# Performance work log

Hardware: AMD Instinct MI355X
Metric: run time of the kernel (lower is better)

## Reference

```python
import jax, jax.numpy as jnp
import numpy as np

NEG_SLOPE = 0.2
N_NODES = 50000


def _gat_layer(x, src, dst, invalid, W, al, ar, b):
    # x: [N, Fin]; src/dst: [E] (self-loops appended); invalid: [E] bool
    N = x.shape[0]
    H, F = al.shape
    z = (x @ W).reshape(N, H, F)                       # [N,H,F]
    el = jnp.sum(z * al[None], axis=-1)                # [N,H]
    er = jnp.sum(z * ar[None], axis=-1)                # [N,H]
    e = el[src] + er[dst]                              # [E,H]
    e = jnp.where(e > 0, e, NEG_SLOPE * e)             # LeakyReLU(0.2)
    e = jnp.where(invalid[:, None], -jnp.inf, e)       # removed self-loop edges
    # edge softmax per destination node (every node has a self-loop -> max finite)
    m = jax.ops.segment_max(e, dst, num_segments=N)    # [N,H]
    ex = jnp.exp(e - m[dst])
    ex = jnp.where(invalid[:, None], 0.0, ex)
    s = jax.ops.segment_sum(ex, dst, num_segments=N)   # [N,H]
    alpha = ex / s[dst]                                # [E,H]
    msg = z[src] * alpha[:, :, None]                   # [E,H,F]
    out = jax.ops.segment_sum(msg, dst, num_segments=N)  # [N,H,F]
    out = out + b.reshape(1, H, F)
    return jax.nn.elu(out)


def _with_self_loops(src, dst):
    N = N_NODES
    loop = jnp.arange(N, dtype=src.dtype)
    invalid = jnp.concatenate([src == dst, jnp.zeros(N, dtype=bool)])
    return jnp.concatenate([src, loop]), jnp.concatenate([dst, loop]), invalid


def setup_inputs() -> dict:
    key = jax.random.key(0)
    ks = jax.random.split(key, 12)
    N, Fin, H0, F0, H1, C = N_NODES, 256, 4, 32, 1, 40
    E = 800000
    sc = lambda k, shp, fan: jax.random.normal(k, shp, jnp.float32) * (1.0 / np.sqrt(fan))
    return {
        "x": jax.random.normal(ks[0], (N, Fin), jnp.float32),
        "src": jax.random.randint(ks[1], (E,), 0, N, jnp.int32),
        "dst": jax.random.randint(ks[2], (E,), 0, N, jnp.int32),
        "W0": sc(ks[3], (Fin, H0 * F0), Fin),
        "al0": sc(ks[4], (H0, F0), F0),
        "ar0": sc(ks[5], (H0, F0), F0),
        "b0": jnp.zeros((H0 * F0,), jnp.float32),
        "W1": sc(ks[6], (H0 * F0, H1 * C), H0 * F0),
        "al1": sc(ks[7], (H1, C), C),
        "ar1": sc(ks[8], (H1, C), C),
        "b1": jnp.zeros((C,), jnp.float32),
    }


def reference(x, src, dst, W0, al0, ar0, b0, W1, al1, ar1, b1):
    s, d, invalid = _with_self_loops(src, dst)
    h = _gat_layer(x, s, d, invalid, W0, al0, ar0, b0)   # [N,4,32]
    h = h.reshape(h.shape[0], -1)                        # flatten(1) -> [N,128]
    h = _gat_layer(h, s, d, invalid, W1, al1, ar1, b1)   # [N,1,40]
    return h.mean(axis=1)                                # mean over heads -> [N,40]
```

## Files before the change

kernel.cpp:

```cpp
#include <hip/hip_runtime.h>
#include <stdint.h>

#define NN 50000
#define EE 800000
#define CAP 48
#define NXCD 8
#define NPX 6250
#define EPB 2048
#define NCHUNK 391

typedef __bf16 bf16x8 __attribute__((ext_vector_type(8)));
typedef float  f32x4  __attribute__((ext_vector_type(4)));

__device__ __forceinline__ float bflo(unsigned int w){ union{unsigned int i;float f;}c; c.i=w<<16; return c.f; }
__device__ __forceinline__ float bfhi(unsigned int w){ union{unsigned int i;float f;}c; c.i=w&0xFFFF0000u; return c.f; }
__device__ __forceinline__ bf16x8 bf8_zero(){
  bf16x8 v;
  #pragma unroll
  for (int j=0;j<8;++j) v[j]=(__bf16)0.f;
  return v;
}

__global__ __launch_bounds__(256) void k_prepW0(const float* __restrict__ W0,
                                                __bf16* __restrict__ Wg){
  int tg = blockIdx.x*256 + threadIdx.x;
  if (tg >= 4096) return;
  int k8 = tg >> 7, n = tg & 127;
  bf16x8 v;
  #pragma unroll
  for (int j=0;j<8;++j) v[j] = (__bf16)W0[(k8*8+j)*128 + n];
  *(bf16x8*)(Wg + ((size_t)(k8*128 + n))*8) = v;
}

__global__ __launch_bounds__(256) void k_gemm0(const float* __restrict__ x,
    const __bf16* __restrict__ Wg, const float* __restrict__ al0, const float* __restrict__ ar0,
    __bf16* __restrict__ z0b, float* __restrict__ el0, float* __restrict__ er0,
    int* __restrict__ cursor, int* __restrict__ csrv){
  const int tid = threadIdx.x;
  const int wv = tid >> 6, ln = tid & 63, q = ln >> 4, mr = ln & 15;
  const int nhalf = wv & 1, mhalf = wv >> 1;
  const int m0w = blockIdx.x*64 + mhalf*32;
  const int n0w = nhalf*64;
  f32x4 acc[2][4];
  #pragma unroll
  for (int mt=0;mt<2;++mt)
    #pragma unroll
    for (int nt=0;nt<4;++nt) acc[mt][nt] = (f32x4){0.f,0.f,0.f,0.f};
  const bool av0 = (m0w + mr) < NN;
  const bool av1 = (m0w + 16 + mr) < NN;
  const float* xr0 = x + (size_t)(m0w + mr)*256;
  const float* xr1 = x + (size_t)(m0w + 16 + mr)*256;
  #pragma unroll
  for (int kc=0;kc<8;++kc){
    int ko = kc*32 + q*8;
    bf16x8 a0 = bf8_zero(), a1 = bf8_zero();
    if (av0){
      float4 p = *(const float4*)(xr0 + ko);
      float4 p2 = *(const float4*)(xr0 + ko + 4);
      a0[0]=(__bf16)p.x; a0[1]=(__bf16)p.y; a0[2]=(__bf16)p.z; a0[3]=(__bf16)p.w;
      a0[4]=(__bf16)p2.x; a0[5]=(__bf16)p2.y; a0[6]=(__bf16)p2.z; a0[7]=(__bf16)p2.w;
    }
    if (av1){
      float4 p = *(const float4*)(xr1 + ko);
      float4 p2 = *(const float4*)(xr1 + ko + 4);
      a1[0]=(__bf16)p.x; a1[1]=(__bf16)p.y; a1[2]=(__bf16)p.z; a1[3]=(__bf16)p.w;
      a1[4]=(__bf16)p2.x; a1[5]=(__bf16)p2.y; a1[6]=(__bf16)p2.z; a1[7]=(__bf16)p2.w;
    }
    const __bf16* wb = Wg + ((size_t)((kc*4+q)*128 + n0w + mr))*8;
    #pragma unroll
    for (int nt=0;nt<4;++nt){
      bf16x8 bf = *(const bf16x8*)(wb + (size_t)nt*16*8);
      acc[0][nt] = __builtin_amdgcn_mfma_f32_16x16x32_bf16(a0, bf, acc[0][nt], 0,0,0);
      acc[1][nt] = __builtin_amdgcn_mfma_f32_16x16x32_bf16(a1, bf, acc[1][nt], 0,0,0);
    }
  }
  float alv[4], arv[4];
  #pragma unroll
  for (int nt=0;nt<4;++nt){ int c = n0w + nt*16 + mr; alv[nt]=al0[c]; arv[nt]=ar0[c]; }
  #pragma unroll
  for (int mt=0;mt<2;++mt){
    #pragma unroll
    for (int r=0;r<4;++r){
      int grow = m0w + mt*16 + q*4 + r;
      if (grow < NN){
        #pragma unroll
        for (int nt=0;nt<4;++nt)
          z0b[(size_t)grow*128 + n0w + nt*16 + mr] = (__bf16)acc[mt][nt][r];
      }
      float pl0 = acc[mt][0][r]*alv[0] + acc[mt][1][r]*alv[1];
      float pr0 = acc[mt][0][r]*arv[0] + acc[mt][1][r]*arv[1];
      float pl1 = acc[mt][2][r]*alv[2] + acc[mt][3][r]*alv[3];
      float pr1 = acc[mt][2][r]*arv[2] + acc[mt][3][r]*arv[3];
      #pragma unroll
      for (int off=1; off<16; off<<=1){
        pl0 += __shfl_xor(pl0, off, 16); pr0 += __shfl_xor(pr0, off, 16);
        pl1 += __shfl_xor(pl1, off, 16); pr1 += __shfl_xor(pr1, off, 16);
      }
      if (mr==0 && grow<NN){
        el0[grow*4 + 2*nhalf]   = pl0; er0[grow*4 + 2*nhalf]   = pr0;
        el0[grow*4 + 2*nhalf+1] = pl1; er0[grow*4 + 2*nhalf+1] = pr1;
        if (nhalf==0){ csrv[(size_t)grow*CAP] = grow; cursor[grow] = 1; }
      }
    }
  }
}

__global__ __launch_bounds__(256) void k_scatter(const int* __restrict__ src,
    const int* __restrict__ dst, int* __restrict__ cursor, int* __restrict__ csrv){
  const int xcd = blockIdx.x & 7;
  const int chunk = blockIdx.x >> 3;
  const int lo = xcd*NPX, hi = lo + NPX;
  int e = chunk*EPB + threadIdx.x;
  #pragma unroll
  for (int it=0; it<EPB/256; ++it, e += 256){
    if (e < EE){
      int d = dst[e];
      if (d >= lo && d < hi){
        int s = src[e];
        unsigned int inv = (s==d) ? 0x80000000u : 0u;
        int pos = atomicAdd(&cursor[d], 1);
        csrv[(size_t)d*CAP + pos] = (int)((unsigned int)s | inv);
      }
    }
  }
}

__global__ __launch_bounds__(256) void k_agg0(const unsigned short* __restrict__ z0b,
    const float* __restrict__ el0, const float* __restrict__ er0,
    const int* __restrict__ cursor, const int* __restrict__ csrv,
    const float* __restrict__ b0, unsigned short* __restrict__ hb){
  int lane = threadIdx.x & 63;
  int i = __builtin_amdgcn_readfirstlane(blockIdx.x*4 + (threadIdx.x >> 6));
  int h1 = lane >> 4;
  int lane2 = lane << 1;
  const float erv = er0[(size_t)i*4 + h1];
  float ax=0.f, ay=0.f, s=0.f;
  int p = i*CAP, pe = p + cursor[i];
  for (; p+8<=pe; p+=8){
    int4 va = *(const int4*)(csrv + p);
    int4 vb = *(const int4*)(csrv + p + 4);
    int v[8] = {va.x,va.y,va.z,va.w,vb.x,vb.y,vb.z,vb.w};
    float el[8];
    #pragma unroll
    for (int j=0;j<8;++j) el[j] = el0[(size_t)(v[j]&0x7FFFFFFF)*4 + h1];
    unsigned int zw[8];
    #pragma unroll
    for (int j=0;j<8;++j)
      zw[j] = *(const unsigned int*)(z0b + (size_t)(v[j]&0x7FFFFFFF)*128 + lane2);
    #pragma unroll
    for (int j=0;j<8;++j){
      float e = el[j] + erv;
      e = fmaxf(e, 0.2f*e);
      float w = (v[j] < 0) ? 0.f : __expf(e);
      s += w; ax = fmaf(w, bflo(zw[j]), ax); ay = fmaf(w, bfhi(zw[j]), ay);
    }
  }
  for (; p+4<=pe; p+=4){
    int4 va = *(const int4*)(csrv + p);
    int v[4] = {va.x,va.y,va.z,va.w};
    float el[4];
    #pragma unroll
    for (int j=0;j<4;++j) el[j] = el0[(size_t)(v[j]&0x7FFFFFFF)*4 + h1];
    unsigned int zw[4];
    #pragma unroll
    for (int j=0;j<4;++j)
      zw[j] = *(const unsigned int*)(z0b + (size_t)(v[j]&0x7FFFFFFF)*128 + lane2);
    #pragma unroll
    for (int j=0;j<4;++j){
      float e = el[j] + erv;
      e = fmaxf(e, 0.2f*e);
      float w = (v[j] < 0) ? 0.f : __expf(e);
      s += w; ax = fmaf(w, bflo(zw[j]), ax); ay = fmaf(w, bfhi(zw[j]), ay);
    }
  }
  for (; p<pe; ++p){
    int v = csrv[p];
    int u = v & 0x7FFFFFFF;
    float e = el0[(size_t)u*4 + h1] + erv;
    e = fmaxf(e, 0.2f*e);
    float w = (v < 0) ? 0.f : __expf(e);
    unsigned int zw = *(const unsigned int*)(z0b + (size_t)u*128 + lane2);
    s += w; ax = fmaf(w, bflo(zw), ax); ay = fmaf(w, bfhi(zw), ay);
  }
  float inv = 1.f/s;
  float ox = ax*inv + b0[lane*2], oy = ay*inv + b0[lane*2+1];
  ox = ox>0.f?ox:__expf(ox)-1.f; oy = oy>0.f?oy:__expf(oy)-1.f;
  union { __bf16 b[2]; unsigned int u; } pk;
  pk.b[0]=(__bf16)ox; pk.b[1]=(__bf16)oy;
  *(unsigned int*)(hb + (size_t)i*128 + lane2) = pk.u;
}

__global__ __launch_bounds__(256) void k_gemm1(const __bf16* __restrict__ hb,
    const float* __restrict__ W1, const float* __restrict__ al1, const float* __restrict__ ar1,
    __bf16* __restrict__ z1b, float* __restrict__ el1, float* __restrict__ er1){
  __shared__ __bf16 Blds[16][48][8];
  const int tid = threadIdx.x;
  for (int t=tid; t<16*48*8; t+=256) (&Blds[0][0][0])[t] = (__bf16)0.f;
  __syncthreads();
  for (int t=tid; t<5120; t+=256){
    int k = t/40, n = t - k*40;
    Blds[k>>3][n][k&7] = (__bf16)W1[t];
  }
  __syncthreads();
  const int wm = tid >> 6, ln = tid & 63, q = ln >> 4, mr = ln & 15;
  const int m0 = blockIdx.x*64 + wm*16;
  const int arow = m0 + mr;
  const bool av = (arow < NN);
  f32x4 acc[3];
  #pragma unroll
  for (int nt=0;nt<3;++nt) acc[nt] = (f32x4){0.f,0.f,0.f,0.f};
  #pragma unroll
  for (int kc=0;kc<4;++kc){
    bf16x8 af = bf8_zero();
    if (av) af = *(const bf16x8*)(hb + (size_t)arow*128 + kc*32 + q*8);
    #pragma unroll
    for (int nt=0;nt<3;++nt){
      bf16x8 bf = *(const bf16x8*)&Blds[kc*4+q][nt*16+mr][0];
      acc[nt] = __builtin_amdgcn_mfma_f32_16x16x32_bf16(af, bf, acc[nt], 0,0,0);
    }
  }
  float alv[3], arv[3];
  #pragma unroll
  for (int nt=0;nt<3;++nt){
    int c = nt*16+mr;
    alv[nt] = (c<40) ? al1[c] : 0.f;
    arv[nt] = (c<40) ? ar1[c] : 0.f;
  }
  #pragma unroll
  for (int r=0;r<4;++r){
    int grow = m0 + q*4 + r;
    if (grow < NN){
      #pragma unroll
      for (int nt=0;nt<3;++nt){
        int c = nt*16+mr;
        if (c < 40) z1b[(size_t)grow*40 + c] = (__bf16)acc[nt][r];
      }
    }
    float pl = acc[0][r]*alv[0] + acc[1][r]*alv[1] + acc[2][r]*alv[2];
    float pr = acc[0][r]*arv[0] + acc[1][r]*arv[1] + acc[2][r]*arv[2];
    #pragma unroll
    for (int off=1; off<16; off<<=1){ pl += __shfl_xor(pl, off, 16); pr += __shfl_xor(pr, off, 16); }
    if (mr==0 && grow<NN){ el1[grow]=pl; er1[grow]=pr; }
  }
}

__global__ __launch_bounds__(256) void k_agg1(const unsigned short* __restrict__ z1b,
    const float* __restrict__ el1, const float* __restrict__ er1,
    const int* __restrict__ cursor, const int* __restrict__ csrv,
    const float* __restrict__ b1, float* __restrict__ out){
  int lane = threadIdx.x & 63;
  int i = __builtin_amdgcn_readfirstlane(blockIdx.x*4 + (threadIdx.x >> 6));
  int fl = (lane < 20) ? (lane<<1) : 0;
  const float erv = er1[i];
  float ax=0.f, ay=0.f, s=0.f;
  int p = i*CAP, pe = p + cursor[i];
  for (; p+8<=pe; p+=8){
    int4 va = *(const int4*)(csrv + p);
    int4 vb = *(const int4*)(csrv + p + 4);
    int v[8] = {va.x,va.y,va.z,va.w,vb.x,vb.y,vb.z,vb.w};
    float el[8];
    #pragma unroll
    for (int j=0;j<8;++j) el[j] = el1[v[j]&0x7FFFFFFF];
    unsigned int zw[8];
    #pragma unroll
    for (int j=0;j<8;++j)
      zw[j] = *(const unsigned int*)(z1b + (size_t)(v[j]&0x7FFFFFFF)*40 + fl);
    #pragma unroll
    for (int j=0;j<8;++j){
      float e = el[j] + erv;
      e = fmaxf(e, 0.2f*e);
      float w = (v[j] < 0) ? 0.f : __expf(e);
      s += w; ax = fmaf(w, bflo(zw[j]), ax); ay = fmaf(w, bfhi(zw[j]), ay);
    }
  }
  for (; p+4<=pe; p+=4){
    int4 va = *(const int4*)(csrv + p);
    int v[4] = {va.x,va.y,va.z,va.w};
    float el[4];
    #pragma unroll
    for (int j=0;j<4;++j) el[j] = el1[v[j]&0x7FFFFFFF];
    unsigned int zw[4];
    #pragma unroll
    for (int j=0;j<4;++j)
      zw[j] = *(const unsigned int*)(z1b + (size_t)(v[j]&0x7FFFFFFF)*40 + fl);
    #pragma unroll
    for (int j=0;j<4;++j){
      float e = el[j] + erv;
      e = fmaxf(e, 0.2f*e);
      float w = (v[j] < 0) ? 0.f : __expf(e);
      s += w; ax = fmaf(w, bflo(zw[j]), ax); ay = fmaf(w, bfhi(zw[j]), ay);
    }
  }
  for (; p<pe; ++p){
    int v = csrv[p];
    int u = v & 0x7FFFFFFF;
    float e = el1[u] + erv;
    e = fmaxf(e, 0.2f*e);
    float w = (v < 0) ? 0.f : __expf(e);
    unsigned int zw = *(const unsigned int*)(z1b + (size_t)u*40 + fl);
    s += w; ax = fmaf(w, bflo(zw), ax); ay = fmaf(w, bfhi(zw), ay);
  }
  if (lane < 20){
    float inv = 1.f/s;
    float ox = ax*inv + b1[lane*2], oy = ay*inv + b1[lane*2+1];
    ox = ox>0.f?ox:__expf(ox)-1.f; oy = oy>0.f?oy:__expf(oy)-1.f;
    *(float2*)(out + (size_t)i*40 + (lane<<1)) = make_float2(ox, oy);
  }
}

extern "C" void kernel_launch(void* const* d_in, const int* in_sizes, int n_in,
                              void* d_out, int out_size, void* d_ws, size_t ws_size,
                              hipStream_t stream){
  const float* x   = (const float*)d_in[0];
  const int*   src = (const int*)d_in[1];
  const int*   dst = (const int*)d_in[2];
  const float* W0  = (const float*)d_in[3];
  const float* al0 = (const float*)d_in[4];
  const float* ar0 = (const float*)d_in[5];
  const float* b0  = (const float*)d_in[6];
  const float* W1  = (const float*)d_in[7];
  const float* al1 = (const float*)d_in[8];
  const float* ar1 = (const float*)d_in[9];
  const float* b1  = (const float*)d_in[10];
  float* out = (float*)d_out;

  __bf16* z0b = (__bf16*)d_ws;
  __bf16* hb  = z0b + (size_t)NN*128;
  __bf16* z1b = hb  + (size_t)NN*128;
  __bf16* Wg  = z1b + (size_t)NN*40;
  float* el0 = (float*)(Wg + 32768);
  float* er0 = el0 + (size_t)NN*4;
  float* el1 = er0 + (size_t)NN*4;
  float* er1 = el1 + NN;
  int* cursor = (int*)(er1 + NN);
  int* csrv   = cursor + NN;

  k_prepW0 <<<16, 256, 0, stream>>>(W0, Wg);
  k_gemm0<<<(NN+63)/64, 256, 0, stream>>>(x, Wg, al0, ar0, z0b, el0, er0, cursor, csrv);
  k_scatter<<<NCHUNK*NXCD, 256, 0, stream>>>(src, dst, cursor, csrv);
  k_agg0 <<<NN/4, 256, 0, stream>>>((const unsigned short*)z0b, el0, er0, cursor, csrv, b0, (unsigned short*)hb);
  k_gemm1<<<(NN+63)/64, 256, 0, stream>>>(hb, W1, al1, ar1, z1b, el1, er1);
  k_agg1 <<<NN/4, 256, 0, stream>>>((const unsigned short*)z1b, el1, er1, cursor, csrv, b1, out);
}
```

Before: 239.4 us.

## Fuse edge scatter into layer-0 GEMM launch and move CSR init to prep

```diff
diff --git a/kernel.cpp b/kernel.cpp
--- a/kernel.cpp
+++ b/kernel.cpp
@@ -8,6 +8,7 @@
 #define NPX 6250
 #define EPB 2048
 #define NCHUNK 391
+#define GB0 782
 
 typedef __bf16 bf16x8 __attribute__((ext_vector_type(8)));
 typedef float  f32x4  __attribute__((ext_vector_type(4)));
@@ -21,21 +22,48 @@
   return v;
 }
 
-__global__ __launch_bounds__(256) void k_prepW0(const float* __restrict__ W0,
-                                                __bf16* __restrict__ Wg){
+__global__ __launch_bounds__(256) void k_prep(const float* __restrict__ W0,
+                                              __bf16* __restrict__ Wg,
+                                              int* __restrict__ cursor,
+                                              int* __restrict__ csrv){
   int tg = blockIdx.x*256 + threadIdx.x;
-  if (tg >= 4096) return;
-  int k8 = tg >> 7, n = tg & 127;
-  bf16x8 v;
-  #pragma unroll
-  for (int j=0;j<8;++j) v[j] = (__bf16)W0[(k8*8+j)*128 + n];
-  *(bf16x8*)(Wg + ((size_t)(k8*128 + n))*8) = v;
-}
-
-__global__ __launch_bounds__(256) void k_gemm0(const float* __restrict__ x,
+  if (tg < 4096){
+    int k8 = tg >> 7, n = tg & 127;
+    bf16x8 v;
+    #pragma unroll
+    for (int j=0;j<8;++j) v[j] = (__bf16)W0[(k8*8+j)*128 + n];
+    *(bf16x8*)(Wg + ((size_t)(k8*128 + n))*8) = v;
+  }
+  if (tg < NN){
+    cursor[tg] = 1;
+    csrv[(size_t)tg*CAP] = tg;
+  }
+}
+
+__global__ __launch_bounds__(256) void k_gemm0_scatter(const float* __restrict__ x,
     const __bf16* __restrict__ Wg, const float* __restrict__ al0, const float* __restrict__ ar0,
     __bf16* __restrict__ z0b, float* __restrict__ el0, float* __restrict__ er0,
+    const int* __restrict__ src, const int* __restrict__ dst,
     int* __restrict__ cursor, int* __restrict__ csrv){
+  if (blockIdx.x >= GB0){
+    const int xcd = blockIdx.x & 7;
+    const int chunk = (blockIdx.x - GB0) >> 3;
+    const int lo = xcd*NPX, hi = lo + NPX;
+    int e = chunk*EPB + threadIdx.x;
+    #pragma unroll
+    for (int it=0; it<EPB/256; ++it, e += 256){
+      if (e < EE){
+        int d = dst[e];
+        if (d >= lo && d < hi){
+          int s = src[e];
+          unsigned int inv = (s==d) ? 0x80000000u : 0u;
+          int pos = atomicAdd(&cursor[d], 1);
+          csrv[(size_t)d*CAP + pos] = (int)((unsigned int)s | inv);
+        }
+      }
+    }
+    return;
+  }
   const int tid = threadIdx.x;
   const int wv = tid >> 6, ln = tid & 63, q = ln >> 4, mr = ln & 15;
   const int nhalf = wv & 1, mhalf = wv >> 1;
@@ -99,27 +127,6 @@
       if (mr==0 && grow<NN){
         el0[grow*4 + 2*nhalf]   = pl0; er0[grow*4 + 2*nhalf]   = pr0;
         el0[grow*4 + 2*nhalf+1] = pl1; er0[grow*4 + 2*nhalf+1] = pr1;
-        if (nhalf==0){ csrv[(size_t)grow*CAP] = grow; cursor[grow] = 1; }
-      }
-    }
-  }
-}
-
-__global__ __launch_bounds__(256) void k_scatter(const int* __restrict__ src,
-    const int* __restrict__ dst, int* __restrict__ cursor, int* __restrict__ csrv){
-  const int xcd = blockIdx.x & 7;
-  const int chunk = blockIdx.x >> 3;
-  const int lo = xcd*NPX, hi = lo + NPX;
-  int e = chunk*EPB + threadIdx.x;
-  #pragma unroll
-  for (int it=0; it<EPB/256; ++it, e += 256){
-    if (e < EE){
-      int d = dst[e];
-      if (d >= lo && d < hi){
-        int s = src[e];
-        unsigned int inv = (s==d) ? 0x80000000u : 0u;
-        int pos = atomicAdd(&cursor[d], 1);
-        csrv[(size_t)d*CAP + pos] = (int)((unsigned int)s | inv);
       }
     }
   }
@@ -335,9 +342,9 @@
   int* cursor = (int*)(er1 + NN);
   int* csrv   = cursor + NN;
 
-  k_prepW0 <<<16, 256, 0, stream>>>(W0, Wg);
-  k_gemm0<<<(NN+63)/64, 256, 0, stream>>>(x, Wg, al0, ar0, z0b, el0, er0, cursor, csrv);
-  k_scatter<<<NCHUNK*NXCD, 256, 0, stream>>>(src, dst, cursor, csrv);
+  k_prep<<<(NN+255)/256, 256, 0, stream>>>(W0, Wg, cursor, csrv);
+  k_gemm0_scatter<<<GB0 + NCHUNK*NXCD, 256, 0, stream>>>(x, Wg, al0, ar0, z0b, el0, er0,
+                                                         src, dst, cursor, csrv);
   k_agg0 <<<NN/4, 256, 0, stream>>>((const unsigned short*)z0b, el0, er0, cursor, csrv, b0, (unsigned short*)hb);
   k_gemm1<<<(NN+63)/64, 256, 0, stream>>>(hb, W1, al1, ar1, z1b, el1, er1);
   k_agg1 <<<NN/4, 256, 0, stream>>>((const unsigned short*)z1b, el1, er1, cursor, csrv, b1, out);
```

New measurement: 225.8 us. 5.7% less time.
